# Kernel tuning notes

Measured on AMD Instinct MI355X. Metric: run time of the kernel, lower is better.

Reference implementation:

```python
import jax, jax.numpy as jnp
import numpy as np

N_HEAD, D_MODEL, D_HEAD = 16, 1024, 64
SCALE = 1.0 / (D_HEAD ** 0.5)
LN_EPS = 1e-5


def _rel_shift(x):
    # x: [b, n, i, j] -> Transformer-XL relative shift
    b, n, i, j = x.shape
    x_padded = jnp.pad(x, ((0, 0), (0, 0), (0, 0), (1, 0)))  # [b,n,i,j+1]
    x_padded = x_padded.reshape(b, n, j + 1, i)
    return x_padded[:, :, 1:, :].reshape(b, n, i, j)


def _layer_norm(x, g, b):
    mu = jnp.mean(x, axis=-1, keepdims=True)
    var = jnp.mean(jnp.square(x - mu), axis=-1, keepdims=True)
    return (x - mu) * jax.lax.rsqrt(var + LN_EPS) * g + b


def setup_inputs() -> dict:
    key = jax.random.key(0)
    ks = jax.random.split(key, 16)
    qlen, bsz = 2048, 2
    d = D_MODEL
    h = N_HEAD * D_HEAD
    s = 0.02
    inp = {
        "w": jax.random.normal(ks[0], (qlen, bsz, d), jnp.float32),
        "r": jax.random.normal(ks[1], (qlen, d), jnp.float32),
        "r_w_bias": jax.random.normal(ks[2], (N_HEAD, D_HEAD), jnp.float32) * s,
        "r_r_bias": jax.random.normal(ks[3], (N_HEAD, D_HEAD), jnp.float32) * s,
        "Wq": jax.random.normal(ks[4], (d, h), jnp.float32) * s,
        "bq": jnp.zeros((h,), jnp.float32),
        "Wk": jax.random.normal(ks[5], (d, h), jnp.float32) * s,
        "bk": jnp.zeros((h,), jnp.float32),
        "Wv": jax.random.normal(ks[6], (d, h), jnp.float32) * s,
        "bv": jnp.zeros((h,), jnp.float32),
        "Wr": jax.random.normal(ks[7], (d, h), jnp.float32) * s,
        "br": jnp.zeros((h,), jnp.float32),
        "Wo": jax.random.normal(ks[8], (h, d), jnp.float32) * s,
        "bo": jnp.zeros((d,), jnp.float32),
        "ln_g": jnp.ones((d,), jnp.float32),
        "ln_b": jnp.zeros((d,), jnp.float32),
        # causal mask: True = masked (future positions)
        "attn_mask": jnp.triu(jnp.ones((qlen, qlen), dtype=bool), k=1),
    }
    return inp


def reference(w, r, r_w_bias, r_r_bias, Wq, bq, Wk, bk, Wv, bv, Wr, br, Wo, bo, ln_g, ln_b, attn_mask):
    qlen, bsz, _ = w.shape
    rlen = r.shape[0]
    # projections (post-lnorm path: project raw w)
    q = (w @ Wq + bq).reshape(qlen, bsz, N_HEAD, D_HEAD)
    k = (w @ Wk + bk).reshape(qlen, bsz, N_HEAD, D_HEAD)
    v = (w @ Wv + bv).reshape(qlen, bsz, N_HEAD, D_HEAD)
    r_k = (r @ Wr + br).reshape(rlen, N_HEAD, D_HEAD)

    AC = jnp.einsum('ibnd,jbnd->bnij', q + r_w_bias, k)
    BD = jnp.einsum('ibnd,jnd->bnij', q + r_r_bias, r_k)
    BD = _rel_shift(BD)
    attn_score = SCALE * (AC + BD)
    attn_score = jnp.where(attn_mask[None, None, :, :], -jnp.inf, attn_score)

    attn_prob = jax.nn.softmax(attn_score, axis=3)
    attn_vec = jnp.einsum('bnij,jbnd->ibnd', attn_prob, v)
    attn_vec = attn_vec.reshape(qlen, bsz, N_HEAD * D_HEAD)
    attn_out = attn_vec @ Wo + bo
    return _layer_norm(w + attn_out, ln_g, ln_b)
```

## Files before the change

### kernel.cpp

```cpp
#include <hip/hip_runtime.h>
#include <math.h>

#define L 2048
#define BSZ 2
#define NH 16
#define DH 64
#define DM 1024
#define GK 1024
#define SCALE_F 0.125f

#define PSLOT 4160

typedef __attribute__((ext_vector_type(8))) __bf16 bf16x8;
typedef __attribute__((ext_vector_type(4))) __bf16 bf16x4;
typedef __attribute__((ext_vector_type(4))) float f32x4;

__global__ __launch_bounds__(256)
void cast2_f32_bf16(const float* __restrict__ a, int na4,
                    const float* __restrict__ b, int nb4,
                    __bf16* __restrict__ da, __bf16* __restrict__ db_)
{
    int i = blockIdx.x * 256 + threadIdx.x;
    int stride = gridDim.x * 256;
    int tot = na4 + nb4;
    for (; i < tot; i += stride) {
        const float4* s; bf16x4* d; int idx;
        if (i < na4) { s = (const float4*)a; d = (bf16x4*)da; idx = i; }
        else         { s = (const float4*)b; d = (bf16x4*)db_; idx = i - na4; }
        float4 v = s[idx];
        bf16x4 o = { (__bf16)v.x, (__bf16)v.y, (__bf16)v.z, (__bf16)v.w };
        d[idx] = o;
    }
}

__global__ __launch_bounds__(256)
void transpose_w5(const float* s0, const float* s1, const float* s2,
                  const float* s3, const float* s4,
                  __bf16* d0, __bf16* d1, __bf16* d2, __bf16* d3, __bf16* d4)
{
    const float* srcs[5] = { s0, s1, s2, s3, s4 };
    __bf16*      dsts[5] = { d0, d1, d2, d3, d4 };
    const float* src = srcs[blockIdx.z];
    __bf16*      dst = dsts[blockIdx.z];
    __shared__ float tile[32][33];
    const int tx = threadIdx.x & 31, ty = threadIdx.x >> 5;
    const int x0 = blockIdx.x * 32, y0 = blockIdx.y * 32;
    #pragma unroll
    for (int i = 0; i < 32; i += 8)
        tile[ty + i][tx] = src[(size_t)(y0 + ty + i) * 1024 + x0 + tx];
    __syncthreads();
    #pragma unroll
    for (int i = 0; i < 32; i += 8)
        dst[(size_t)(x0 + ty + i) * 1024 + y0 + tx] = (__bf16)tile[tx][ty + i];
}

__global__ __launch_bounds__(256)
void gemm_bf16(const __bf16* __restrict__ A0, const __bf16* __restrict__ A1,
               const __bf16* __restrict__ B0, const __bf16* __restrict__ B1,
               int sched,
               __bf16* __restrict__ o0, __bf16* __restrict__ o1,
               __bf16* __restrict__ o2, __bf16* __restrict__ o3,
               __bf16* __restrict__ o4,
               const float* __restrict__ b0, const float* __restrict__ b1,
               const float* __restrict__ b2, const float* __restrict__ b3,
               const float* __restrict__ rwbf, const float* __restrict__ rrbf,
               float* __restrict__ of)
{
    __shared__ __bf16 As[128 * 64];
    __shared__ __bf16 Bs[128 * 64];

    const __bf16 *A, *Bt;
    int mode, bm, bn;
    if (sched == 0) {
        int id = blockIdx.x;
        if (id < 768) { A = A0; Bt = B0; mode = 0; bm = (id & 31) * 128; bn = (id >> 5) * 128; }
        else { id -= 768; A = A1; Bt = B1; mode = 1; bm = (id & 15) * 128; bn = (id >> 4) * 128; }
    } else {
        A = A0; Bt = B0; mode = 2; bm = blockIdx.x * 128; bn = blockIdx.y * 128;
    }

    const int t    = threadIdx.x;
    const int w    = t >> 6;
    const int lane = t & 63;
    const int row16 = lane & 15;
    const int kgrp  = lane >> 4;
    const int wr = w >> 1, wc = w & 1;

    f32x4 acc[4][4];
    #pragma unroll
    for (int mi = 0; mi < 4; ++mi)
        #pragma unroll
        for (int ni = 0; ni < 4; ++ni)
            acc[mi][ni] = (f32x4){0.f, 0.f, 0.f, 0.f};

    for (int k0 = 0; k0 < GK; k0 += 64) {
        __syncthreads();
        #pragma unroll
        for (int it = 0; it < 4; ++it) {
            const int lin = (it * 256 + t) * 16;
            const int row = lin >> 7;
            const int kb  = lin & 127;
            const char* ga = (const char*)(A + (size_t)(bm + row) * GK + k0) + kb;
            __builtin_amdgcn_global_load_lds(
                (const __attribute__((address_space(1))) void*)ga,
                (__attribute__((address_space(3))) void*)((char*)As + lin), 16, 0, 0);
            const char* gb = (const char*)(Bt + (size_t)(bn + row) * GK + k0) + kb;
            __builtin_amdgcn_global_load_lds(
                (const __attribute__((address_space(1))) void*)gb,
                (__attribute__((address_space(3))) void*)((char*)Bs + lin), 16, 0, 0);
        }
        __syncthreads();

        #pragma unroll
        for (int ks = 0; ks < 2; ++ks) {
            bf16x8 af[4], bfr[4];
            #pragma unroll
            for (int mi = 0; mi < 4; ++mi)
                af[mi] = *reinterpret_cast<const bf16x8*>(
                    &As[(wr * 64 + mi * 16 + row16) * 64 + kgrp * 8 + ks * 32]);
            #pragma unroll
            for (int ni = 0; ni < 4; ++ni)
                bfr[ni] = *reinterpret_cast<const bf16x8*>(
                    &Bs[(wc * 64 + ni * 16 + row16) * 64 + kgrp * 8 + ks * 32]);
            #pragma unroll
            for (int mi = 0; mi < 4; ++mi)
                #pragma unroll
                for (int ni = 0; ni < 4; ++ni)
                    acc[mi][ni] = __builtin_amdgcn_mfma_f32_16x16x32_bf16(
                        af[mi], bfr[ni], acc[mi][ni], 0, 0, 0);
        }
    }

    #pragma unroll
    for (int mi = 0; mi < 4; ++mi) {
        #pragma unroll
        for (int ni = 0; ni < 4; ++ni) {
            #pragma unroll
            for (int r = 0; r < 4; ++r) {
                const int row = bm + wr * 64 + mi * 16 + kgrp * 4 + r;
                const int col = bn + wc * 64 + ni * 16 + row16;
                const float val = acc[mi][ni][r];
                if (mode == 0) {
                    const int which = col >> 10, c = col & 1023;
                    const int n = c >> 6, dh = c & 63;
                    const int i = row >> 1, b = row & 1;
                    const size_t idx = (((size_t)(b * NH + n) * L) + i) * DH + dh;
                    if (which == 0) {
                        const float v0 = val + b0[c];
                        o0[idx] = (__bf16)(v0 + rwbf[c]);
                        o1[idx] = (__bf16)(v0 + rrbf[c]);
                    } else if (which == 1) {
                        o2[idx] = (__bf16)(val + b1[c]);
                    } else {
                        o3[idx] = (__bf16)(val + b2[c]);
                    }
                } else if (mode == 1) {
                    const int n = col >> 6, dh = col & 63;
                    o4[((size_t)n * L + row) * DH + dh] = (__bf16)(val + b3[col]);
                } else {
                    of[(size_t)row * DM + col] = val + b0[col];
                }
            }
        }
    }
}

__global__ __launch_bounds__(256, 4)
void attn_partial(const __bf16* __restrict__ qwg, const __bf16* __restrict__ qrg,
                  const __bf16* __restrict__ kg,  const __bf16* __restrict__ vg,
                  const __bf16* __restrict__ rkg, float* __restrict__ P)
{
    __shared__ __bf16 kt [64][72];
    __shared__ __bf16 vtT[64][72];
    __shared__ __bf16 pt [4][16][72];

    int x = blockIdx.x;
    int it, jc;
    if (x < 8)       { it = x;                      jc = 0; }
    else if (x < 24) { int y = x - 8;  it = 8  + (y >> 1); jc = y & 1; }
    else if (x < 48) { int y = x - 24; it = 16 + y / 3;    jc = y - (y / 3) * 3; }
    else             { int y = x - 48; it = 24 + (y >> 2); jc = y & 3; }

    const int t    = threadIdx.x;
    const int w    = t >> 6;
    const int lane = t & 63;
    const int row16 = lane & 15;
    const int kgrp  = lane >> 4;

    const int bh = blockIdx.y;
    const int n  = bh & (NH - 1);
    const int i0 = it * 64;
    const int i0w = i0 + w * 16;
    const int jstart = jc * 512;
    const int jend   = min(jstart + 512, i0 + 64);

    const __bf16* qwb = qwg + (size_t)bh * L * DH;
    const __bf16* qrb = qrg + (size_t)bh * L * DH;
    const __bf16* kb  = kg  + (size_t)bh * L * DH;
    const __bf16* vb  = vg  + (size_t)bh * L * DH;
    const __bf16* rkb = rkg + (size_t)n  * L * DH;

    bf16x8 qwf[2], qrf[2];
    #pragma unroll
    for (int ks = 0; ks < 2; ++ks) {
        size_t off = (size_t)(i0w + row16) * DH + kgrp * 8 + ks * 32;
        qwf[ks] = *reinterpret_cast<const bf16x8*>(qwb + off);
        qrf[ks] = *reinterpret_cast<const bf16x8*>(qrb + off);
    }

    float l_run[4] = {0.f, 0.f, 0.f, 0.f};
    f32x4 O[4];
    #pragma unroll
    for (int cb = 0; cb < 4; ++cb) O[cb] = (f32x4){0.f, 0.f, 0.f, 0.f};

    for (int j0 = jstart; j0 < jend; j0 += 64) {
        __syncthreads();

        {
            int j  = t >> 2;
            int d0 = (t & 3) * 16;
            bf16x8 ka  = *reinterpret_cast<const bf16x8*>(kb + (size_t)(j0 + j) * DH + d0);
            bf16x8 kb2 = *reinterpret_cast<const bf16x8*>(kb + (size_t)(j0 + j) * DH + d0 + 8);
            *reinterpret_cast<bf16x8*>(&kt[j][d0])     = ka;
            *reinterpret_cast<bf16x8*>(&kt[j][d0 + 8]) = kb2;
            bf16x8 va  = *reinterpret_cast<const bf16x8*>(vb + (size_t)(j0 + j) * DH + d0);
            bf16x8 vb2 = *reinterpret_cast<const bf16x8*>(vb + (size_t)(j0 + j) * DH + d0 + 8);
            #pragma unroll
            for (int kk = 0; kk < 8; ++kk) {
                vtT[d0 + kk][j]     = va[kk];
                vtT[d0 + 8 + kk][j] = vb2[kk];
            }
        }
        __syncthreads();

        f32x4 ac[4];
        #pragma unroll
        for (int cb = 0; cb < 4; ++cb) ac[cb] = (f32x4){0.f, 0.f, 0.f, 0.f};
        #pragma unroll
        for (int ks = 0; ks < 2; ++ks)
            #pragma unroll
            for (int cb = 0; cb < 4; ++cb) {
                bf16x8 kf = *reinterpret_cast<const bf16x8*>(&kt[16 * cb + row16][kgrp * 8 + ks * 32]);
                ac[cb] = __builtin_amdgcn_mfma_f32_16x16x32_bf16(qwf[ks], kf, ac[cb], 0, 0, 0);
            }

        f32x4 db[5];
        #pragma unroll
        for (int cb = 0; cb < 5; ++cb) db[cb] = (f32x4){0.f, 0.f, 0.f, 0.f};
        const int pw0 = (L - 1) + j0 - (i0w + 15);
        #pragma unroll
        for (int ks = 0; ks < 2; ++ks)
            #pragma unroll
            for (int cb = 0; cb < 5; ++cb) {
                int p = pw0 + 16 * cb + row16;
                p = p > (L - 1) ? (L - 1) : p;
                bf16x8 rf = *reinterpret_cast<const bf16x8*>(
                    rkb + (size_t)p * DH + kgrp * 8 + ks * 32);
                db[cb] = __builtin_amdgcn_mfma_f32_16x16x32_bf16(qrf[ks], rf, db[cb], 0, 0, 0);
            }

        #pragma unroll
        for (int r = 0; r < 4; ++r) {
            const int ri = kgrp * 4 + r;
            const int i_glob = i0w + ri;
            const int u  = row16 + 15 - ri;
            const int lo = u & 15;
            const int hi = u >> 4;
            const int srclane = (lane & 48) | lo;
            float T[5];
            #pragma unroll
            for (int c2 = 0; c2 < 5; ++c2)
                T[c2] = __shfl(db[c2][r], srclane, 64);
            float rsum = 0.f;
            #pragma unroll
            for (int cb = 0; cb < 4; ++cb) {
                const int jj = 16 * cb + row16;
                float bd = hi ? T[cb + 1] : T[cb];
                float s = SCALE_F * (ac[cb][r] + bd);
                if (j0 + jj > i_glob) s = -INFINITY;
                float p = __expf(s);
                pt[w][ri][jj] = (__bf16)p;
                rsum += p;
            }
            #pragma unroll
            for (int off = 1; off < 16; off <<= 1)
                rsum += __shfl_xor(rsum, off);
            l_run[r] += rsum;
        }

        #pragma unroll
        for (int ks = 0; ks < 2; ++ks) {
            bf16x8 pf = *reinterpret_cast<const bf16x8*>(&pt[w][row16][kgrp * 8 + ks * 32]);
            #pragma unroll
            for (int cb = 0; cb < 4; ++cb) {
                bf16x8 vf = *reinterpret_cast<const bf16x8*>(&vtT[16 * cb + row16][kgrp * 8 + ks * 32]);
                O[cb] = __builtin_amdgcn_mfma_f32_16x16x32_bf16(pf, vf, O[cb], 0, 0, 0);
            }
        }
    }

    float* Pb = P + ((size_t)bh * 32 + it) * PSLOT;
    #pragma unroll
    for (int r = 0; r < 4; ++r) {
        const int row = w * 16 + kgrp * 4 + r;
        #pragma unroll
        for (int cb = 0; cb < 4; ++cb)
            atomicAdd(&Pb[row * 64 + 16 * cb + row16], O[cb][r]);
        if (row16 == 0)
            atomicAdd(&Pb[4096 + row], l_run[r]);
    }
}

__global__ __launch_bounds__(256)
void attn_reduce(const float* __restrict__ P, __bf16* __restrict__ av)
{
    const int bh = blockIdx.y;
    const int it = blockIdx.x;
    const int n = bh & (NH - 1), b = bh >> 4;
    const float* Pb = P + ((size_t)bh * 32 + it) * PSLOT;
    const int t = threadIdx.x;
    const int row = t >> 2;
    const int c0 = (t & 3) * 16;
    const float inv = 1.0f / Pb[4096 + row];
    const int i_glob = it * 64 + row;
    __bf16* dst = av + (size_t)(i_glob * BSZ + b) * (NH * DH) + n * DH + c0;
    #pragma unroll
    for (int v4 = 0; v4 < 4; ++v4) {
        float4 o = *reinterpret_cast<const float4*>(&Pb[row * 64 + c0 + v4 * 4]);
        bf16x4 ov = { (__bf16)(o.x * inv), (__bf16)(o.y * inv),
                      (__bf16)(o.z * inv), (__bf16)(o.w * inv) };
        *reinterpret_cast<bf16x4*>(dst + v4 * 4) = ov;
    }
}

__global__ __launch_bounds__(256)
void ln_fused(const float* __restrict__ w, const float* __restrict__ ao,
              const float* __restrict__ g, const float* __restrict__ bb,
              float* __restrict__ out)
{
    const int row = blockIdx.x;
    const float* wr = w  + (size_t)row * DM;
    const float* ar = ao + (size_t)row * DM;
    const int t = threadIdx.x;
    float x[4];
    float s = 0.f;
    #pragma unroll
    for (int j = 0; j < 4; ++j) {
        int c = t + j * 256;
        x[j] = wr[c] + ar[c];
        s += x[j];
    }
    __shared__ float red[4];
    #pragma unroll
    for (int off = 1; off < 64; off <<= 1) s += __shfl_xor(s, off);
    int wid = t >> 6, lane = t & 63;
    if (lane == 0) red[wid] = s;
    __syncthreads();
    float mu = (red[0] + red[1] + red[2] + red[3]) * (1.0f / DM);
    float ss = 0.f;
    #pragma unroll
    for (int j = 0; j < 4; ++j) { float d = x[j] - mu; ss += d * d; }
    #pragma unroll
    for (int off = 1; off < 64; off <<= 1) ss += __shfl_xor(ss, off);
    __syncthreads();
    if (lane == 0) red[wid] = ss;
    __syncthreads();
    float var = (red[0] + red[1] + red[2] + red[3]) * (1.0f / DM);
    float rstd = rsqrtf(var + 1e-5f);
    #pragma unroll
    for (int j = 0; j < 4; ++j) {
        int c = t + j * 256;
        out[(size_t)row * DM + c] = (x[j] - mu) * rstd * g[c] + bb[c];
    }
}

extern "C" void kernel_launch(void* const* d_in, const int* in_sizes, int n_in,
                              void* d_out, int out_size, void* d_ws, size_t ws_size,
                              hipStream_t stream)
{
    (void)in_sizes; (void)n_in; (void)out_size; (void)ws_size;
    const float* w   = (const float*)d_in[0];
    const float* r   = (const float*)d_in[1];
    const float* rwb = (const float*)d_in[2];
    const float* rrb = (const float*)d_in[3];
    const float* Wq  = (const float*)d_in[4];
    const float* bq  = (const float*)d_in[5];
    const float* Wk  = (const float*)d_in[6];
    const float* bk  = (const float*)d_in[7];
    const float* Wv  = (const float*)d_in[8];
    const float* bv  = (const float*)d_in[9];
    const float* Wr  = (const float*)d_in[10];
    const float* br  = (const float*)d_in[11];
    const float* Wo  = (const float*)d_in[12];
    const float* bo  = (const float*)d_in[13];
    const float* lng = (const float*)d_in[14];
    const float* lnb = (const float*)d_in[15];
    float* out = (float*)d_out;

    const size_t NQ = (size_t)BSZ * NH * L * DH;
    const size_t PN = (size_t)BSZ * NH * 32 * PSLOT;
    char* wsb = (char*)d_ws;
    __bf16* w_bf    = (__bf16*)wsb;  wsb += (size_t)2 * L * DM * 2;
    __bf16* r_bf    = (__bf16*)wsb;  wsb += (size_t)L * DM * 2;
    __bf16* wqkv_t  = (__bf16*)wsb;  wsb += (size_t)3 * DM * DM * 2;
    __bf16* wr_t    = (__bf16*)wsb;  wsb += (size_t)DM * DM * 2;
    __bf16* wo_t    = (__bf16*)wsb;  wsb += (size_t)DM * DM * 2;
    __bf16* qw_ws   = (__bf16*)wsb;  wsb += NQ * 2;
    __bf16* qr_ws   = (__bf16*)wsb;  wsb += NQ * 2;
    __bf16* k_ws    = (__bf16*)wsb;  wsb += NQ * 2;
    __bf16* v_ws    = (__bf16*)wsb;  wsb += NQ * 2;
    __bf16* rk_ws   = (__bf16*)wsb;  wsb += (size_t)NH * L * DH * 2;
    __bf16* av_ws   = (__bf16*)wsb;  wsb += NQ * 2;
    float*  P_ws    = (float*)wsb;
    float*  ao_ws   = P_ws;

    dim3 blk(256);
    hipMemsetAsync(P_ws, 0, PN * sizeof(float), stream);

    cast2_f32_bf16<<<dim3(1536), blk, 0, stream>>>(
        w, (2 * L * DM) / 4, r, (L * DM) / 4, w_bf, r_bf);
    transpose_w5<<<dim3(32, 32, 5), blk, 0, stream>>>(
        Wq, Wk, Wv, Wr, Wo,
        wqkv_t, wqkv_t + (size_t)DM * DM, wqkv_t + (size_t)2 * DM * DM, wr_t, wo_t);

    gemm_bf16<<<dim3(896), blk, 0, stream>>>(w_bf, r_bf, wqkv_t, wr_t, 0,
        qw_ws, qr_ws, k_ws, v_ws, rk_ws, bq, bk, bv, br, rwb, rrb, nullptr);

    attn_partial<<<dim3(80, BSZ * NH), blk, 0, stream>>>(
        qw_ws, qr_ws, k_ws, v_ws, rk_ws, P_ws);
    attn_reduce<<<dim3(32, BSZ * NH), blk, 0, stream>>>(P_ws, av_ws);

    gemm_bf16<<<dim3(32, 8), blk, 0, stream>>>(av_ws, nullptr, wo_t, nullptr, 1,
        nullptr, nullptr, nullptr, nullptr, nullptr, bo, nullptr, nullptr, nullptr,
        nullptr, nullptr, ao_ws);

    ln_fused<<<dim3(L * BSZ), blk, 0, stream>>>(w, ao_ws, lng, lnb, out);
}
```

Measured before the change: 421.4 us.

## Pre-transpose V and read K/V fragments directly from global memory in attention

Adds a separate kernel that transposes V per (batch, head) into a d-major layout. The attention kernel then drops its shared-memory K and V^T staging and both per-tile barriers, and loads MFMA operand fragments for K and V^T straight from global memory. This removes the scattered LDS transpose writes and the synchronisation. In exchange it adds a kernel launch and an extra pass over V, and each wave now reloads K/V from global or cache instead of sharing one staged tile.

```diff
diff --git a/kernel.cpp b/kernel.cpp
--- a/kernel.cpp
+++ b/kernel.cpp
@@ -52,6 +52,23 @@
     #pragma unroll
     for (int i = 0; i < 32; i += 8)
         dst[(size_t)(x0 + ty + i) * 1024 + y0 + tx] = (__bf16)tile[tx][ty + i];
+}
+
+__global__ __launch_bounds__(256)
+void transpose_v(const __bf16* __restrict__ src, __bf16* __restrict__ dst)
+{
+    __shared__ __bf16 tile[32][34];
+    const __bf16* s = src + (size_t)blockIdx.z * L * DH;
+    __bf16*       d = dst + (size_t)blockIdx.z * L * DH;
+    const int tx = threadIdx.x & 31, ty = threadIdx.x >> 5;
+    const int j0 = blockIdx.x * 32, d0 = blockIdx.y * 32;
+    #pragma unroll
+    for (int i = 0; i < 32; i += 8)
+        tile[ty + i][tx] = s[(size_t)(j0 + ty + i) * DH + d0 + tx];
+    __syncthreads();
+    #pragma unroll
+    for (int i = 0; i < 32; i += 8)
+        d[(size_t)(d0 + ty + i) * L + j0 + tx] = tile[tx][ty + i];
 }
 
 __global__ __launch_bounds__(256)
@@ -167,11 +184,9 @@
 
 __global__ __launch_bounds__(256, 4)
 void attn_partial(const __bf16* __restrict__ qwg, const __bf16* __restrict__ qrg,
-                  const __bf16* __restrict__ kg,  const __bf16* __restrict__ vg,
+                  const __bf16* __restrict__ kg,  const __bf16* __restrict__ vTg,
                   const __bf16* __restrict__ rkg, float* __restrict__ P)
 {
-    __shared__ __bf16 kt [64][72];
-    __shared__ __bf16 vtT[64][72];
     __shared__ __bf16 pt [4][16][72];
 
     int x = blockIdx.x;
@@ -197,7 +212,7 @@
     const __bf16* qwb = qwg + (size_t)bh * L * DH;
     const __bf16* qrb = qrg + (size_t)bh * L * DH;
     const __bf16* kb  = kg  + (size_t)bh * L * DH;
-    const __bf16* vb  = vg  + (size_t)bh * L * DH;
+    const __bf16* vTb = vTg + (size_t)bh * L * DH;
     const __bf16* rkb = rkg + (size_t)n  * L * DH;
 
     bf16x8 qwf[2], qrf[2];
@@ -214,25 +229,6 @@
     for (int cb = 0; cb < 4; ++cb) O[cb] = (f32x4){0.f, 0.f, 0.f, 0.f};
 
     for (int j0 = jstart; j0 < jend; j0 += 64) {
-        __syncthreads();
-
-        {
-            int j  = t >> 2;
-            int d0 = (t & 3) * 16;
-            bf16x8 ka  = *reinterpret_cast<const bf16x8*>(kb + (size_t)(j0 + j) * DH + d0);
-            bf16x8 kb2 = *reinterpret_cast<const bf16x8*>(kb + (size_t)(j0 + j) * DH + d0 + 8);
-            *reinterpret_cast<bf16x8*>(&kt[j][d0])     = ka;
-            *reinterpret_cast<bf16x8*>(&kt[j][d0 + 8]) = kb2;
-            bf16x8 va  = *reinterpret_cast<const bf16x8*>(vb + (size_t)(j0 + j) * DH + d0);
-            bf16x8 vb2 = *reinterpret_cast<const bf16x8*>(vb + (size_t)(j0 + j) * DH + d0 + 8);
-            #pragma unroll
-            for (int kk = 0; kk < 8; ++kk) {
-                vtT[d0 + kk][j]     = va[kk];
-                vtT[d0 + 8 + kk][j] = vb2[kk];
-            }
-        }
-        __syncthreads();
-
         f32x4 ac[4];
         #pragma unroll
         for (int cb = 0; cb < 4; ++cb) ac[cb] = (f32x4){0.f, 0.f, 0.f, 0.f};
@@ -240,7 +236,8 @@
         for (int ks = 0; ks < 2; ++ks)
             #pragma unroll
             for (int cb = 0; cb < 4; ++cb) {
-                bf16x8 kf = *reinterpret_cast<const bf16x8*>(&kt[16 * cb + row16][kgrp * 8 + ks * 32]);
+                bf16x8 kf = *reinterpret_cast<const bf16x8*>(
+                    kb + (size_t)(j0 + 16 * cb + row16) * DH + kgrp * 8 + ks * 32);
                 ac[cb] = __builtin_amdgcn_mfma_f32_16x16x32_bf16(qwf[ks], kf, ac[cb], 0, 0, 0);
             }
 
@@ -293,7 +290,8 @@
             bf16x8 pf = *reinterpret_cast<const bf16x8*>(&pt[w][row16][kgrp * 8 + ks * 32]);
             #pragma unroll
             for (int cb = 0; cb < 4; ++cb) {
-                bf16x8 vf = *reinterpret_cast<const bf16x8*>(&vtT[16 * cb + row16][kgrp * 8 + ks * 32]);
+                bf16x8 vf = *reinterpret_cast<const bf16x8*>(
+                    vTb + (size_t)(16 * cb + row16) * L + j0 + kgrp * 8 + ks * 32);
                 O[cb] = __builtin_amdgcn_mfma_f32_16x16x32_bf16(pf, vf, O[cb], 0, 0, 0);
             }
         }
@@ -409,6 +407,7 @@
     __bf16* qr_ws   = (__bf16*)wsb;  wsb += NQ * 2;
     __bf16* k_ws    = (__bf16*)wsb;  wsb += NQ * 2;
     __bf16* v_ws    = (__bf16*)wsb;  wsb += NQ * 2;
+    __bf16* vT_ws   = (__bf16*)wsb;  wsb += NQ * 2;
     __bf16* rk_ws   = (__bf16*)wsb;  wsb += (size_t)NH * L * DH * 2;
     __bf16* av_ws   = (__bf16*)wsb;  wsb += NQ * 2;
     float*  P_ws    = (float*)wsb;
@@ -426,8 +425,10 @@
     gemm_bf16<<<dim3(896), blk, 0, stream>>>(w_bf, r_bf, wqkv_t, wr_t, 0,
         qw_ws, qr_ws, k_ws, v_ws, rk_ws, bq, bk, bv, br, rwb, rrb, nullptr);
 
+    transpose_v<<<dim3(L / 32, DH / 32, BSZ * NH), blk, 0, stream>>>(v_ws, vT_ws);
+
     attn_partial<<<dim3(80, BSZ * NH), blk, 0, stream>>>(
-        qw_ws, qr_ws, k_ws, v_ws, rk_ws, P_ws);
+        qw_ws, qr_ws, k_ws, vT_ws, rk_ws, P_ws);
     attn_reduce<<<dim3(32, BSZ * NH), blk, 0, stream>>>(P_ws, av_ws);
 
     gemm_bf16<<<dim3(32, 8), blk, 0, stream>>>(av_ws, nullptr, wo_t, nullptr, 1,
```

Result: slower. 521.6 us (+23.8%).
